# Performance work log

Hardware: AMD Instinct MI355X
Metric: run time of the kernel (lower is better)

Reference implementation:

```python
import jax, jax.numpy as jnp
import numpy as np

EPS = 1e-5
NUM_GROUPS = 8


def setup_inputs() -> dict:
    key = jax.random.key(0)
    ks = jax.random.split(key, 8)
    B, C, H, W = 4, 64, 64, 64
    scale_w = 1.0 / np.sqrt(C)  # roughly xavier scale for [C,C]
    return {
        "x": jax.random.normal(ks[0], (B, C, H, W), dtype=jnp.float32),
        "gamma": jnp.ones((C,), dtype=jnp.float32),
        "beta": jnp.zeros((C,), dtype=jnp.float32),
        "Wq": jax.random.normal(ks[1], (C, C), dtype=jnp.float32) * scale_w,
        "bq": jnp.zeros((C,), dtype=jnp.float32),
        "Wk": jax.random.normal(ks[2], (C, C), dtype=jnp.float32) * scale_w,
        "bk": jnp.zeros((C,), dtype=jnp.float32),
        "Wv": jax.random.normal(ks[3], (C, C), dtype=jnp.float32) * scale_w,
        "bv": jnp.zeros((C,), dtype=jnp.float32),
        "Wp": jax.random.normal(ks[4], (C, C), dtype=jnp.float32) * scale_w,
        "bp": jnp.zeros((C,), dtype=jnp.float32),
    }


def _group_norm(x, gamma, beta):
    # x: [B, C, H, W]; normalize over (C//G, H, W) within each of G groups
    B, C, H, W = x.shape
    xg = x.reshape(B, NUM_GROUPS, -1)
    mean = jnp.mean(xg, axis=-1, keepdims=True)
    var = jnp.var(xg, axis=-1, keepdims=True)
    xn = ((xg - mean) * jax.lax.rsqrt(var + EPS)).reshape(B, C, H, W)
    return xn * gamma[None, :, None, None] + beta[None, :, None, None]


def reference(x, gamma, beta, Wq, bq, Wk, bk, Wv, bv, Wp, bp):
    B, C, H, W = x.shape
    N = H * W
    xn = _group_norm(x, gamma, beta).reshape(B, C, N)  # [B, C, N]
    # 1x1 convs == per-pixel linear maps over channels
    q = jnp.einsum('oc,bcn->bon', Wq, xn) + bq[None, :, None]  # [B, C, N]
    k = jnp.einsum('oc,bcn->bon', Wk, xn) + bk[None, :, None]
    v = jnp.einsum('oc,bcn->bon', Wv, xn) + bv[None, :, None]
    scale = 1.0 / jnp.sqrt(jnp.asarray(C, dtype=x.dtype))
    attn = jnp.einsum('bcn,bcm->bnm', q, k) * scale  # [B, N, N]
    attn = jax.nn.softmax(attn, axis=-1)
    out = jnp.einsum('bnm,bcm->bcn', attn, v)  # [B, C, N]
    out = jnp.einsum('oc,bcn->bon', Wp, out) + bp[None, :, None]
    return x + out.reshape(B, C, H, W)
```

## Files before the change

### kernel.cpp

```cpp
#include <hip/hip_runtime.h>
#include <math.h>

#define B_ 4
#define C_ 64
#define N_ 4096

typedef unsigned short u16;
typedef __attribute__((ext_vector_type(8))) short bf16x8;
typedef __attribute__((ext_vector_type(4))) float f32x4;
typedef __attribute__((ext_vector_type(16))) float f32x16;
typedef __attribute__((ext_vector_type(2))) int i32x2;

__device__ __forceinline__ u16 f2bf(float f) {
    unsigned u = __float_as_uint(f);
    u += 0x7fff + ((u >> 16) & 1);
    return (u16)(u >> 16);
}
__device__ __forceinline__ float bf2f(u16 h) {
    return __uint_as_float(((unsigned)h) << 16);
}

__global__ __launch_bounds__(256) void gn_reduce(const float* __restrict__ x,
                                                 float* __restrict__ partials) {
    int bg = blockIdx.x >> 3, chunk = blockIdx.x & 7;
    const float4* xv = (const float4*)(x + (size_t)bg * 32768 + (size_t)chunk * 4096);
    float s = 0.f, ss = 0.f;
    #pragma unroll
    for (int k = 0; k < 4; k++) {
        float4 v = xv[threadIdx.x + 256 * k];
        s += v.x + v.y + v.z + v.w;
        ss += v.x * v.x + v.y * v.y + v.z * v.z + v.w * v.w;
    }
    #pragma unroll
    for (int off = 1; off < 64; off <<= 1) {
        s += __shfl_xor(s, off);
        ss += __shfl_xor(ss, off);
    }
    __shared__ float red[2][4];
    int w = threadIdx.x >> 6;
    if ((threadIdx.x & 63) == 0) { red[0][w] = s; red[1][w] = ss; }
    __syncthreads();
    if (threadIdx.x == 0) {
        s = red[0][0] + red[0][1] + red[0][2] + red[0][3];
        ss = red[1][0] + red[1][1] + red[1][2] + red[1][3];
        partials[bg * 16 + chunk * 2] = s;
        partials[bg * 16 + chunk * 2 + 1] = ss;
    }
}

__global__ __launch_bounds__(256) void qkv_kernel(
    const float* __restrict__ x, const float* __restrict__ gamma,
    const float* __restrict__ beta, const float* __restrict__ partials,
    const float* __restrict__ Wq, const float* __restrict__ bq,
    const float* __restrict__ Wk, const float* __restrict__ bk,
    const float* __restrict__ Wv, const float* __restrict__ bv,
    u16* __restrict__ Qo, u16* __restrict__ Ko, u16* __restrict__ Vt) {
    __shared__ __align__(16) u16 wt[3][64][64];
    __shared__ __align__(16) u16 xs[64][64];
    __shared__ __align__(16) u16 odt[64][72];

    const int b = blockIdx.x >> 6;
    const int nt = blockIdx.x & 63;
    const int tid = threadIdx.x;
    const float* Ws[3] = {Wq, Wk, Wv};
    const float* bs[3] = {bq, bk, bv};

    {
        const int rw = tid >> 2, qd = tid & 3;
        #pragma unroll
        for (int s = 0; s < 3; s++) {
            const float4* wsrc = (const float4*)(Ws[s] + rw * 64 + qd * 16);
            float4 f0 = wsrc[0], f1 = wsrc[1], f2 = wsrc[2], f3 = wsrc[3];
            u16 pk[16];
            pk[0]=f2bf(f0.x); pk[1]=f2bf(f0.y); pk[2]=f2bf(f0.z); pk[3]=f2bf(f0.w);
            pk[4]=f2bf(f1.x); pk[5]=f2bf(f1.y); pk[6]=f2bf(f1.z); pk[7]=f2bf(f1.w);
            pk[8]=f2bf(f2.x); pk[9]=f2bf(f2.y); pk[10]=f2bf(f2.z); pk[11]=f2bf(f2.w);
            pk[12]=f2bf(f3.x); pk[13]=f2bf(f3.y); pk[14]=f2bf(f3.z); pk[15]=f2bf(f3.w);
            int blk0 = (2 * qd) ^ (rw & 7), blk1 = (2 * qd + 1) ^ (rw & 7);
            *(uint4*)&wt[s][rw][blk0 * 8] = *(uint4*)&pk[0];
            *(uint4*)&wt[s][rw][blk1 * 8] = *(uint4*)&pk[8];
        }
    }
    {
        const int c = tid >> 2, px0 = (tid & 3) * 16;
        const int g = c >> 3, bg = b * 8 + g;
        float s = 0.f, ss = 0.f;
        #pragma unroll
        for (int i = 0; i < 8; i++) {
            s += partials[bg * 16 + i * 2];
            ss += partials[bg * 16 + i * 2 + 1];
        }
        float mean = s * (1.f / 32768.f);
        float var = ss * (1.f / 32768.f) - mean * mean;
        float rstd = rsqrtf(var + 1e-5f);
        float ga = gamma[c] * rstd;
        float bb = beta[c] - mean * ga;
        const float4* xp = (const float4*)(x + ((size_t)(b * 64 + c)) * N_ + nt * 64 + px0);
        float4 q0 = xp[0], q1 = xp[1], q2 = xp[2], q3 = xp[3];
        float vals[16] = {q0.x,q0.y,q0.z,q0.w, q1.x,q1.y,q1.z,q1.w,
                          q2.x,q2.y,q2.z,q2.w, q3.x,q3.y,q3.z,q3.w};
        #pragma unroll
        for (int e = 0; e < 16; e++) {
            int px = px0 + e;
            xs[px][((c >> 3) ^ (px & 7)) * 8 + (c & 7)] = f2bf(vals[e] * ga + bb);
        }
    }
    __syncthreads();

    const int lane = tid & 63, w = tid >> 6;
    const int lr = lane & 15, lg = lane >> 4;
    const f32x4 zz = {0.f, 0.f, 0.f, 0.f};
    const int sa0 = (lg ^ (lr & 7)) * 8, sa1 = ((4 | lg) ^ (lr & 7)) * 8;

    #pragma unroll
    for (int s = 0; s < 3; s++) {
        bf16x8 a0 = *(const bf16x8*)&wt[s][w * 16 + lr][sa0];
        bf16x8 a1 = *(const bf16x8*)&wt[s][w * 16 + lr][sa1];
        float bias[4];
        #pragma unroll
        for (int r = 0; r < 4; r++) bias[r] = bs[s][w * 16 + lg * 4 + r];
        #pragma unroll
        for (int pt = 0; pt < 4; pt++) {
            bf16x8 b0 = *(const bf16x8*)&xs[pt * 16 + lr][sa0];
            bf16x8 b1 = *(const bf16x8*)&xs[pt * 16 + lr][sa1];
            f32x4 acc = __builtin_amdgcn_mfma_f32_16x16x32_bf16(a0, b0, zz, 0, 0, 0);
            acc = __builtin_amdgcn_mfma_f32_16x16x32_bf16(a1, b1, acc, 0, 0, 0);
            if (s == 0) {
                #pragma unroll
                for (int r = 0; r < 4; r++)
                    odt[pt * 16 + lr][w * 16 + lg * 4 + r] = f2bf((acc[r] + bias[r]) * 0.18033688f);
            } else if (s == 1) {
                #pragma unroll
                for (int r = 0; r < 4; r++)
                    odt[pt * 16 + lr][w * 16 + lg * 4 + r] = f2bf(acc[r] + bias[r]);
            } else {
                #pragma unroll
                for (int r = 0; r < 4; r++)
                    odt[w * 16 + lg * 4 + r][pt * 16 + lr] = f2bf(acc[r] + bias[r]);
            }
        }
        __syncthreads();
        if (s < 2) {
            u16* dst = (s == 0 ? Qo : Ko) + ((size_t)(b * N_ + nt * 64)) * 64;
            #pragma unroll
            for (int k2 = 0; k2 < 2; k2++) {
                int c = tid + k2 * 256;
                int px = c >> 3, blk = c & 7;
                *(uint4*)(dst + (size_t)px * 64 + blk * 8) = *(const uint4*)&odt[px][blk * 8];
            }
        } else {
            #pragma unroll
            for (int k2 = 0; k2 < 2; k2++) {
                int c = tid + k2 * 256;
                int co = c >> 3, blk = c & 7;
                *(uint4*)(Vt + ((size_t)(b * 64 + co)) * N_ + nt * 64 + blk * 8) =
                    *(const uint4*)&odt[co][blk * 8];
            }
        }
        __syncthreads();
    }
}

__global__ __launch_bounds__(256, 4) void flash_kernel(
    const u16* __restrict__ Qg, const u16* __restrict__ Kg,
    const u16* __restrict__ Vg, u16* __restrict__ Opart, float* __restrict__ ml,
    int nsplit) {
    __shared__ __align__(16) u16 smem[16384];
    u16* const Ksb0 = smem;
    u16* const Ksb1 = smem + 4096;
    u16* const Vsb0 = smem + 8192;
    u16* const Vsb1 = smem + 12288;

    const int sp = blockIdx.x >> 8;
    const int b  = (blockIdx.x >> 6) & 3;
    const int qt = blockIdx.x & 63;
    const int tid = threadIdx.x;
    const int w = tid >> 6, lane = tid & 63;
    const int l31 = lane & 31, lh = lane >> 5;
    const int qh = w >> 1, kh = w & 1;

    const int per = (nsplit == 4) ? 16 : (nsplit == 3) ? 22 : 32;
    const int kt0 = sp * per;
    const int NT = min(per, 64 - kt0);

    const u16* qptr = Qg + ((size_t)(b * N_ + qt * 64 + qh * 32 + l31)) * 64 + lh * 8;
    bf16x8 q0 = *(const bf16x8*)(qptr);
    bf16x8 q1 = *(const bf16x8*)(qptr + 16);
    bf16x8 q2 = *(const bf16x8*)(qptr + 32);
    bf16x8 q3 = *(const bf16x8*)(qptr + 48);

    const int srow = tid >> 2;
    const int scb  = (tid & 3) * 32;
    const char* Kbase = (const char*)(Kg + (size_t)b * N_ * C_) + (size_t)srow * 128 + scb;
    const char* Vbase = (const char*)(Vg + (size_t)b * C_ * N_) + (size_t)srow * (N_ * 2) + scb;
    const int se0 = srow * 64 + (((scb)      ^ ((srow & 7) << 4)) >> 1);
    const int se1 = srow * 64 + (((scb + 16) ^ ((srow & 7) << 4)) >> 1);

    const int key = kh * 32 + l31;
    int kaoff[4];
    #pragma unroll
    for (int s = 0; s < 4; s++)
        kaoff[s] = key * 64 + (((s * 2 + lh) ^ (key & 7)) << 3);
    int vboff[2][2];
    #pragma unroll
    for (int c = 0; c < 2; c++) {
        int ch = c * 32 + l31;
        #pragma unroll
        for (int s = 0; s < 2; s++)
            vboff[c][s] = ch * 64 + (((kh * 4 + s * 2 + lh) ^ (ch & 7)) << 3);
    }

    {
        uint4 k0a = *(const uint4*)(Kbase + (size_t)kt0 * 8192);
        uint4 k0b = *(const uint4*)(Kbase + (size_t)kt0 * 8192 + 16);
        uint4 v0a = *(const uint4*)(Vbase + kt0 * 128);
        uint4 v0b = *(const uint4*)(Vbase + kt0 * 128 + 16);
        *(uint4*)&Ksb0[se0] = k0a;  *(uint4*)&Ksb0[se1] = k0b;
        *(uint4*)&Vsb0[se0] = v0a;  *(uint4*)&Vsb0[se1] = v0b;
    }
    uint4 ka = *(const uint4*)(Kbase + (size_t)(kt0 + 1) * 8192);
    uint4 kb = *(const uint4*)(Kbase + (size_t)(kt0 + 1) * 8192 + 16);
    uint4 va = *(const uint4*)(Vbase + (kt0 + 1) * 128);
    uint4 vb = *(const uint4*)(Vbase + (kt0 + 1) * 128 + 16);
    __syncthreads();

    f32x16 o0, o1;
    #pragma unroll
    for (int r = 0; r < 16; r++) { o0[r] = 0.f; o1[r] = 0.f; }
    float lsum = 0.f;

    bf16x8 paC0 = {}, paC1 = {};
    bf16x8 vC0 = {}, vC1 = {}, vC2 = {}, vC3 = {};

    for (int t = 0; t < NT; ++t) {
        const int bi = t & 1;
        const u16* ks = bi ? Ksb1 : Ksb0;
        const u16* vs = bi ? Vsb1 : Vsb0;
        u16* kd = bi ? Ksb0 : Ksb1;
        u16* vd = bi ? Vsb0 : Vsb1;

        bf16x8 vN0 = *(const bf16x8*)&vs[vboff[0][0]];
        bf16x8 vN1 = *(const bf16x8*)&vs[vboff[0][1]];
        bf16x8 vN2 = *(const bf16x8*)&vs[vboff[1][0]];
        bf16x8 vN3 = *(const bf16x8*)&vs[vboff[1][1]];

        if (t > 0) {
            __builtin_amdgcn_s_setprio(1);
            o0 = __builtin_amdgcn_mfma_f32_32x32x16_bf16(paC0, vC0, o0, 0, 0, 0);
            o0 = __builtin_amdgcn_mfma_f32_32x32x16_bf16(paC1, vC1, o0, 0, 0, 0);
            o1 = __builtin_amdgcn_mfma_f32_32x32x16_bf16(paC0, vC2, o1, 0, 0, 0);
            o1 = __builtin_amdgcn_mfma_f32_32x32x16_bf16(paC1, vC3, o1, 0, 0, 0);
            __builtin_amdgcn_s_setprio(0);
        }

        f32x16 st;
        #pragma unroll
        for (int r = 0; r < 16; r++) st[r] = 0.f;
        __builtin_amdgcn_s_setprio(1);
        st = __builtin_amdgcn_mfma_f32_32x32x16_bf16(*(const bf16x8*)&ks[kaoff[0]], q0, st, 0, 0, 0);
        st = __builtin_amdgcn_mfma_f32_32x32x16_bf16(*(const bf16x8*)&ks[kaoff[1]], q1, st, 0, 0, 0);
        st = __builtin_amdgcn_mfma_f32_32x32x16_bf16(*(const bf16x8*)&ks[kaoff[2]], q2, st, 0, 0, 0);
        st = __builtin_amdgcn_mfma_f32_32x32x16_bf16(*(const bf16x8*)&ks[kaoff[3]], q3, st, 0, 0, 0);
        __builtin_amdgcn_s_setprio(0);

        #pragma unroll
        for (int r = 0; r < 16; r++) st[r] = exp2f(st[r] - 12.f);
        lsum += (((st[0]+st[1])+(st[2]+st[3])) + ((st[4]+st[5])+(st[6]+st[7])))
              + (((st[8]+st[9])+(st[10]+st[11])) + ((st[12]+st[13])+(st[14]+st[15])));
        unsigned c0,c1,c2,c3,c4,c5,c6,c7;
        asm("v_cvt_pk_bf16_f32 %0, %1, %2" : "=v"(c0) : "v"(st[0]),  "v"(st[1]));
        asm("v_cvt_pk_bf16_f32 %0, %1, %2" : "=v"(c1) : "v"(st[2]),  "v"(st[3]));
        asm("v_cvt_pk_bf16_f32 %0, %1, %2" : "=v"(c2) : "v"(st[4]),  "v"(st[5]));
        asm("v_cvt_pk_bf16_f32 %0, %1, %2" : "=v"(c3) : "v"(st[6]),  "v"(st[7]));
        asm("v_cvt_pk_bf16_f32 %0, %1, %2" : "=v"(c4) : "v"(st[8]),  "v"(st[9]));
        asm("v_cvt_pk_bf16_f32 %0, %1, %2" : "=v"(c5) : "v"(st[10]), "v"(st[11]));
        asm("v_cvt_pk_bf16_f32 %0, %1, %2" : "=v"(c6) : "v"(st[12]), "v"(st[13]));
        asm("v_cvt_pk_bf16_f32 %0, %1, %2" : "=v"(c7) : "v"(st[14]), "v"(st[15]));
        i32x2 r02 = __builtin_amdgcn_permlane32_swap((int)c0, (int)c2, false, false);
        i32x2 r13 = __builtin_amdgcn_permlane32_swap((int)c1, (int)c3, false, false);
        i32x2 r46 = __builtin_amdgcn_permlane32_swap((int)c4, (int)c6, false, false);
        i32x2 r57 = __builtin_amdgcn_permlane32_swap((int)c5, (int)c7, false, false);
        union U { int u[4]; bf16x8 v; };
        U pa0 = {{r02[0], r13[0], r02[1], r13[1]}};
        U pa1 = {{r46[0], r57[0], r46[1], r57[1]}};
        paC0 = pa0.v;
        paC1 = pa1.v;

        if (t < NT - 1) {
            *(uint4*)&kd[se0] = ka;  *(uint4*)&kd[se1] = kb;
            *(uint4*)&vd[se0] = va;  *(uint4*)&vd[se1] = vb;
        }
        __syncthreads();
        if (t < NT - 2) {
            int kt = kt0 + t + 2;
            ka = *(const uint4*)(Kbase + (size_t)kt * 8192);
            kb = *(const uint4*)(Kbase + (size_t)kt * 8192 + 16);
            va = *(const uint4*)(Vbase + kt * 128);
            vb = *(const uint4*)(Vbase + kt * 128 + 16);
        }

        vC0 = vN0; vC1 = vN1; vC2 = vN2; vC3 = vN3;
    }

    o0 = __builtin_amdgcn_mfma_f32_32x32x16_bf16(paC0, vC0, o0, 0, 0, 0);
    o0 = __builtin_amdgcn_mfma_f32_32x32x16_bf16(paC1, vC1, o0, 0, 0, 0);
    o1 = __builtin_amdgcn_mfma_f32_32x32x16_bf16(paC0, vC2, o1, 0, 0, 0);
    o1 = __builtin_amdgcn_mfma_f32_32x32x16_bf16(paC1, vC3, o1, 0, 0, 0);

    float* red = (float*)smem;
    u16* ost = smem + 10240;
    if (kh == 1) {
        float* dst = red + (qh * 64 + lane) * 34;
        #pragma unroll
        for (int r = 0; r < 16; r++) { dst[r] = o0[r]; dst[16 + r] = o1[r]; }
        dst[32] = lsum;
    }
    __syncthreads();
    if (kh == 0) {
        const float* src = red + (qh * 64 + lane) * 34;
        float l2 = lsum + src[32];
        i32x2 rr = __builtin_amdgcn_permlane32_swap(__float_as_int(l2), __float_as_int(l2), false, false);
        float lpart = __int_as_float(lh ? rr[0] : rr[1]);
        float lfull = l2 + lpart;
        #pragma unroll
        for (int r = 0; r < 16; r++) {
            float v0 = o0[r] + src[r];
            float v1 = o1[r] + src[16 + r];
            int ql = qh * 32 + (r & 3) + 8 * (r >> 2) + 4 * lh;
            ost[ql * 64 + l31] = f2bf(v0);
            ost[ql * 64 + 32 + l31] = f2bf(v1);
        }
        if (lane < 32)
            ml[(size_t)sp * 16384 + b * N_ + qt * 64 + qh * 32 + l31] = lfull;
    }
    __syncthreads();
    uint4* op = (uint4*)(Opart + (size_t)sp * 1048576 + ((size_t)(b * N_ + qt * 64)) * 64);
    const uint4* os4 = (const uint4*)ost;
    op[tid] = os4[tid];
    op[tid + 256] = os4[tid + 256];
}

__global__ __launch_bounds__(256) void proj_kernel(
    const u16* __restrict__ Opart, const float* __restrict__ ml,
    const float* __restrict__ Wp, const float* __restrict__ bp,
    const float* __restrict__ x, float* __restrict__ out, int nsplit) {
    __shared__ __align__(16) u16 wp[64][64];
    __shared__ __align__(16) u16 og[64][64];
    const int b = blockIdx.x >> 6;
    const int nt = blockIdx.x & 63;
    const int tid = threadIdx.x;

    {
        const int rw = tid >> 2, qd = tid & 3;
        const float4* wsrc = (const float4*)(Wp + rw * 64 + qd * 16);
        float4 f0 = wsrc[0], f1 = wsrc[1], f2 = wsrc[2], f3 = wsrc[3];
        u16 pk[16];
        pk[0]=f2bf(f0.x); pk[1]=f2bf(f0.y); pk[2]=f2bf(f0.z); pk[3]=f2bf(f0.w);
        pk[4]=f2bf(f1.x); pk[5]=f2bf(f1.y); pk[6]=f2bf(f1.z); pk[7]=f2bf(f1.w);
        pk[8]=f2bf(f2.x); pk[9]=f2bf(f2.y); pk[10]=f2bf(f2.z); pk[11]=f2bf(f2.w);
        pk[12]=f2bf(f3.x); pk[13]=f2bf(f3.y); pk[14]=f2bf(f3.z); pk[15]=f2bf(f3.w);
        int blk0 = (2 * qd) ^ (rw & 7), blk1 = (2 * qd + 1) ^ (rw & 7);
        *(uint4*)&wp[rw][blk0 * 8] = *(uint4*)&pk[0];
        *(uint4*)&wp[rw][blk1 * 8] = *(uint4*)&pk[8];
    }
    {
        #pragma unroll
        for (int k2 = 0; k2 < 2; k2++) {
            int cidx = tid + k2 * 256;
            int px = cidx >> 3, blk = cidx & 7;
            int gpix = b * N_ + nt * 64 + px;
            float lsum = 0.f;
            for (int s = 0; s < nsplit; s++) lsum += ml[(size_t)s * 16384 + gpix];
            float inv = 1.f / lsum;
            float acc8[8] = {0.f,0.f,0.f,0.f,0.f,0.f,0.f,0.f};
            for (int s = 0; s < nsplit; s++) {
                u16 ov[8];
                *(uint4*)ov = *(const uint4*)(Opart + (size_t)s * 1048576 + (size_t)gpix * 64 + blk * 8);
                #pragma unroll
                for (int j = 0; j < 8; j++) acc8[j] += bf2f(ov[j]);
            }
            u16 y[8];
            #pragma unroll
            for (int j = 0; j < 8; j++) y[j] = f2bf(acc8[j] * inv);
            *(uint4*)&og[px][(blk ^ (px & 7)) * 8] = *(uint4*)y;
        }
    }
    __syncthreads();

    const int lane = tid & 63, w = tid >> 6;
    const int lr = lane & 15, lg = lane >> 4;
    const f32x4 zz = {0.f, 0.f, 0.f, 0.f};
    const int sa0 = (lg ^ (lr & 7)) * 8, sa1 = ((4 | lg) ^ (lr & 7)) * 8;

    bf16x8 a0 = *(const bf16x8*)&wp[w * 16 + lr][sa0];
    bf16x8 a1 = *(const bf16x8*)&wp[w * 16 + lr][sa1];
    float bias[4];
    #pragma unroll
    for (int r = 0; r < 4; r++) bias[r] = bp[w * 16 + lg * 4 + r];

    #pragma unroll
    for (int pt = 0; pt < 4; pt++) {
        bf16x8 b0 = *(const bf16x8*)&og[pt * 16 + lr][sa0];
        bf16x8 b1 = *(const bf16x8*)&og[pt * 16 + lr][sa1];
        f32x4 acc = __builtin_amdgcn_mfma_f32_16x16x32_bf16(a0, b0, zz, 0, 0, 0);
        acc = __builtin_amdgcn_mfma_f32_16x16x32_bf16(a1, b1, acc, 0, 0, 0);
        #pragma unroll
        for (int r = 0; r < 4; r++) {
            int cout = w * 16 + lg * 4 + r;
            int px = pt * 16 + lr;
            size_t idx = ((size_t)(b * 64 + cout)) * N_ + nt * 64 + px;
            out[idx] = x[idx] + bias[r] + acc[r];
        }
    }
}

extern "C" void kernel_launch(void* const* d_in, const int* in_sizes, int n_in,
                              void* d_out, int out_size, void* d_ws, size_t ws_size,
                              hipStream_t stream) {
    const float* x     = (const float*)d_in[0];
    const float* gamma = (const float*)d_in[1];
    const float* beta  = (const float*)d_in[2];
    const float* Wq    = (const float*)d_in[3];
    const float* bq    = (const float*)d_in[4];
    const float* Wk    = (const float*)d_in[5];
    const float* bk    = (const float*)d_in[6];
    const float* Wv    = (const float*)d_in[7];
    const float* bv    = (const float*)d_in[8];
    const float* Wp    = (const float*)d_in[9];
    const float* bp    = (const float*)d_in[10];
    float* out = (float*)d_out;

    const size_t elems = (size_t)B_ * N_ * C_;
    const size_t base = 4096 + 262144;
    float* partials = (float*)d_ws;
    float* ml = (float*)((char*)d_ws + 4096);
    u16* Qb = (u16*)((char*)d_ws + base);
    u16* Kb = Qb + elems;
    u16* Vt = Kb + elems;
    u16* Opart = Vt + elems;

    const size_t need4 = base + 3 * elems * 2 + 4 * elems * 2;
    const size_t need3 = base + 3 * elems * 2 + 3 * elems * 2;
    const int nsplit = (ws_size >= need4) ? 4 : (ws_size >= need3) ? 3 : 2;

    gn_reduce<<<256, 256, 0, stream>>>(x, partials);
    qkv_kernel<<<256, 256, 0, stream>>>(x, gamma, beta, partials,
                                        Wq, bq, Wk, bk, Wv, bv, Qb, Kb, Vt);
    flash_kernel<<<nsplit * 256, 256, 0, stream>>>(Qb, Kb, Vt, Opart, ml, nsplit);
    proj_kernel<<<256, 256, 0, stream>>>(Opart, ml, Wp, bp, x, out, nsplit);
}
```

Before: 56.17 us.

## Pre-swizzle K/V into MFMA fragment order and load directly from global

The QKV kernel now writes K and V in a per-tile layout that matches the MFMA operand fragment order, so each lane's bf16x8 operand sits contiguously in global memory. The flash kernel drops the LDS double buffer, swizzle and per-iteration __syncthreads, loads K and V fragments straight into registers, and prefetches the next K tile. The PV MFMAs are no longer deferred by one iteration. This removes LDS traffic and block barriers, but each wave pair now reads K/V tiles redundantly from global or L2 and relies on the cache to hide latency. The K prefetch on the last iteration also reads one tile past the split's range.

```diff
diff --git a/kernel.cpp b/kernel.cpp
--- a/kernel.cpp
+++ b/kernel.cpp
@@ -54,7 +54,7 @@
     const float* __restrict__ Wq, const float* __restrict__ bq,
     const float* __restrict__ Wk, const float* __restrict__ bk,
     const float* __restrict__ Wv, const float* __restrict__ bv,
-    u16* __restrict__ Qo, u16* __restrict__ Ko, u16* __restrict__ Vt) {
+    u16* __restrict__ Qo, u16* __restrict__ Kf, u16* __restrict__ Vf) {
     __shared__ __align__(16) u16 wt[3][64][64];
     __shared__ __align__(16) u16 xs[64][64];
     __shared__ __align__(16) u16 odt[64][72];
@@ -140,36 +140,43 @@
             }
         }
         __syncthreads();
-        if (s < 2) {
-            u16* dst = (s == 0 ? Qo : Ko) + ((size_t)(b * N_ + nt * 64)) * 64;
+        if (s == 0) {
+            u16* dst = Qo + ((size_t)(b * N_ + nt * 64)) * 64;
             #pragma unroll
             for (int k2 = 0; k2 < 2; k2++) {
                 int c = tid + k2 * 256;
                 int px = c >> 3, blk = c & 7;
                 *(uint4*)(dst + (size_t)px * 64 + blk * 8) = *(const uint4*)&odt[px][blk * 8];
             }
-        } else {
+        } else if (s == 1) {
+            u16* dst = Kf + ((size_t)(b * 64 + nt)) * 4096;
             #pragma unroll
             for (int k2 = 0; k2 < 2; k2++) {
-                int c = tid + k2 * 256;
-                int co = c >> 3, blk = c & 7;
-                *(uint4*)(Vt + ((size_t)(b * 64 + co)) * N_ + nt * 64 + blk * 8) =
-                    *(const uint4*)&odt[co][blk * 8];
+                int f = tid + k2 * 256;
+                int khf = f >> 8, sf = (f >> 6) & 3, lhf = (f >> 5) & 1, l31f = f & 31;
+                *(uint4*)(dst + (size_t)f * 8) =
+                    *(const uint4*)&odt[khf * 32 + l31f][(sf * 2 + lhf) * 8];
             }
+        } else {
+            u16* dst = Vf + ((size_t)(b * 64 + nt)) * 4096;
+            #pragma unroll
+            for (int k2 = 0; k2 < 2; k2++) {
+                int f = tid + k2 * 256;
+                int khf = f >> 8, cf = (f >> 7) & 1, s2f = (f >> 6) & 1;
+                int lhf = (f >> 5) & 1, l31f = f & 31;
+                *(uint4*)(dst + (size_t)f * 8) =
+                    *(const uint4*)&odt[cf * 32 + l31f][(khf * 4 + s2f * 2 + lhf) * 8];
+            }
         }
         __syncthreads();
     }
 }
 
 __global__ __launch_bounds__(256, 4) void flash_kernel(
-    const u16* __restrict__ Qg, const u16* __restrict__ Kg,
-    const u16* __restrict__ Vg, u16* __restrict__ Opart, float* __restrict__ ml,
+    const u16* __restrict__ Qg, const u16* __restrict__ Kf,
+    const u16* __restrict__ Vf, u16* __restrict__ Opart, float* __restrict__ ml,
     int nsplit) {
-    __shared__ __align__(16) u16 smem[16384];
-    u16* const Ksb0 = smem;
-    u16* const Ksb1 = smem + 4096;
-    u16* const Vsb0 = smem + 8192;
-    u16* const Vsb1 = smem + 12288;
+    __shared__ __align__(16) u16 smem[14336];
 
     const int sp = blockIdx.x >> 8;
     const int b  = (blockIdx.x >> 6) & 3;
@@ -189,79 +196,41 @@
     bf16x8 q2 = *(const bf16x8*)(qptr + 32);
     bf16x8 q3 = *(const bf16x8*)(qptr + 48);
 
-    const int srow = tid >> 2;
-    const int scb  = (tid & 3) * 32;
-    const char* Kbase = (const char*)(Kg + (size_t)b * N_ * C_) + (size_t)srow * 128 + scb;
-    const char* Vbase = (const char*)(Vg + (size_t)b * C_ * N_) + (size_t)srow * (N_ * 2) + scb;
-    const int se0 = srow * 64 + (((scb)      ^ ((srow & 7) << 4)) >> 1);
-    const int se1 = srow * 64 + (((scb + 16) ^ ((srow & 7) << 4)) >> 1);
-
-    const int key = kh * 32 + l31;
-    int kaoff[4];
-    #pragma unroll
-    for (int s = 0; s < 4; s++)
-        kaoff[s] = key * 64 + (((s * 2 + lh) ^ (key & 7)) << 3);
-    int vboff[2][2];
-    #pragma unroll
-    for (int c = 0; c < 2; c++) {
-        int ch = c * 32 + l31;
-        #pragma unroll
-        for (int s = 0; s < 2; s++)
-            vboff[c][s] = ch * 64 + (((kh * 4 + s * 2 + lh) ^ (ch & 7)) << 3);
-    }
-
-    {
-        uint4 k0a = *(const uint4*)(Kbase + (size_t)kt0 * 8192);
-        uint4 k0b = *(const uint4*)(Kbase + (size_t)kt0 * 8192 + 16);
-        uint4 v0a = *(const uint4*)(Vbase + kt0 * 128);
-        uint4 v0b = *(const uint4*)(Vbase + kt0 * 128 + 16);
-        *(uint4*)&Ksb0[se0] = k0a;  *(uint4*)&Ksb0[se1] = k0b;
-        *(uint4*)&Vsb0[se0] = v0a;  *(uint4*)&Vsb0[se1] = v0b;
-    }
-    uint4 ka = *(const uint4*)(Kbase + (size_t)(kt0 + 1) * 8192);
-    uint4 kb = *(const uint4*)(Kbase + (size_t)(kt0 + 1) * 8192 + 16);
-    uint4 va = *(const uint4*)(Vbase + (kt0 + 1) * 128);
-    uint4 vb = *(const uint4*)(Vbase + (kt0 + 1) * 128 + 16);
-    __syncthreads();
+    const u16* kp = Kf + ((size_t)(b * 64 + kt0)) * 4096 + kh * 2048 + lane * 8;
+    const u16* vp = Vf + ((size_t)(b * 64 + kt0)) * 4096 + kh * 2048 + lane * 8;
+
+    bf16x8 kf0 = *(const bf16x8*)(kp);
+    bf16x8 kf1 = *(const bf16x8*)(kp + 512);
+    bf16x8 kf2 = *(const bf16x8*)(kp + 1024);
+    bf16x8 kf3 = *(const bf16x8*)(kp + 1536);
 
     f32x16 o0, o1;
     #pragma unroll
     for (int r = 0; r < 16; r++) { o0[r] = 0.f; o1[r] = 0.f; }
     float lsum = 0.f;
 
-    bf16x8 paC0 = {}, paC1 = {};
-    bf16x8 vC0 = {}, vC1 = {}, vC2 = {}, vC3 = {};
-
     for (int t = 0; t < NT; ++t) {
-        const int bi = t & 1;
-        const u16* ks = bi ? Ksb1 : Ksb0;
-        const u16* vs = bi ? Vsb1 : Vsb0;
-        u16* kd = bi ? Ksb0 : Ksb1;
-        u16* vd = bi ? Vsb0 : Vsb1;
-
-        bf16x8 vN0 = *(const bf16x8*)&vs[vboff[0][0]];
-        bf16x8 vN1 = *(const bf16x8*)&vs[vboff[0][1]];
-        bf16x8 vN2 = *(const bf16x8*)&vs[vboff[1][0]];
-        bf16x8 vN3 = *(const bf16x8*)&vs[vboff[1][1]];
-
-        if (t > 0) {
-            __builtin_amdgcn_s_setprio(1);
-            o0 = __builtin_amdgcn_mfma_f32_32x32x16_bf16(paC0, vC0, o0, 0, 0, 0);
-            o0 = __builtin_amdgcn_mfma_f32_32x32x16_bf16(paC1, vC1, o0, 0, 0, 0);
-            o1 = __builtin_amdgcn_mfma_f32_32x32x16_bf16(paC0, vC2, o1, 0, 0, 0);
-            o1 = __builtin_amdgcn_mfma_f32_32x32x16_bf16(paC1, vC3, o1, 0, 0, 0);
-            __builtin_amdgcn_s_setprio(0);
-        }
+        const u16* vtp = vp + (size_t)t * 4096;
+        bf16x8 vf0 = *(const bf16x8*)(vtp);
+        bf16x8 vf1 = *(const bf16x8*)(vtp + 512);
+        bf16x8 vf2 = *(const bf16x8*)(vtp + 1024);
+        bf16x8 vf3 = *(const bf16x8*)(vtp + 1536);
 
         f32x16 st;
         #pragma unroll
         for (int r = 0; r < 16; r++) st[r] = 0.f;
         __builtin_amdgcn_s_setprio(1);
-        st = __builtin_amdgcn_mfma_f32_32x32x16_bf16(*(const bf16x8*)&ks[kaoff[0]], q0, st, 0, 0, 0);
-        st = __builtin_amdgcn_mfma_f32_32x32x16_bf16(*(const bf16x8*)&ks[kaoff[1]], q1, st, 0, 0, 0);
-        st = __builtin_amdgcn_mfma_f32_32x32x16_bf16(*(const bf16x8*)&ks[kaoff[2]], q2, st, 0, 0, 0);
-        st = __builtin_amdgcn_mfma_f32_32x32x16_bf16(*(const bf16x8*)&ks[kaoff[3]], q3, st, 0, 0, 0);
+        st = __builtin_amdgcn_mfma_f32_32x32x16_bf16(kf0, q0, st, 0, 0, 0);
+        st = __builtin_amdgcn_mfma_f32_32x32x16_bf16(kf1, q1, st, 0, 0, 0);
+        st = __builtin_amdgcn_mfma_f32_32x32x16_bf16(kf2, q2, st, 0, 0, 0);
+        st = __builtin_amdgcn_mfma_f32_32x32x16_bf16(kf3, q3, st, 0, 0, 0);
         __builtin_amdgcn_s_setprio(0);
+
+        const u16* knp = kp + (size_t)(t + 1) * 4096;
+        kf0 = *(const bf16x8*)(knp);
+        kf1 = *(const bf16x8*)(knp + 512);
+        kf2 = *(const bf16x8*)(knp + 1024);
+        kf3 = *(const bf16x8*)(knp + 1536);
 
         #pragma unroll
         for (int r = 0; r < 16; r++) st[r] = exp2f(st[r] - 12.f);
@@ -283,29 +252,14 @@
         union U { int u[4]; bf16x8 v; };
         U pa0 = {{r02[0], r13[0], r02[1], r13[1]}};
         U pa1 = {{r46[0], r57[0], r46[1], r57[1]}};
-        paC0 = pa0.v;
-        paC1 = pa1.v;
-
-        if (t < NT - 1) {
-            *(uint4*)&kd[se0] = ka;  *(uint4*)&kd[se1] = kb;
-            *(uint4*)&vd[se0] = va;  *(uint4*)&vd[se1] = vb;
-        }
-        __syncthreads();
-        if (t < NT - 2) {
-            int kt = kt0 + t + 2;
-            ka = *(const uint4*)(Kbase + (size_t)kt * 8192);
-            kb = *(const uint4*)(Kbase + (size_t)kt * 8192 + 16);
-            va = *(const uint4*)(Vbase + kt * 128);
-            vb = *(const uint4*)(Vbase + kt * 128 + 16);
-        }
-
-        vC0 = vN0; vC1 = vN1; vC2 = vN2; vC3 = vN3;
-    }
-
-    o0 = __builtin_amdgcn_mfma_f32_32x32x16_bf16(paC0, vC0, o0, 0, 0, 0);
-    o0 = __builtin_amdgcn_mfma_f32_32x32x16_bf16(paC1, vC1, o0, 0, 0, 0);
-    o1 = __builtin_amdgcn_mfma_f32_32x32x16_bf16(paC0, vC2, o1, 0, 0, 0);
-    o1 = __builtin_amdgcn_mfma_f32_32x32x16_bf16(paC1, vC3, o1, 0, 0, 0);
+
+        __builtin_amdgcn_s_setprio(1);
+        o0 = __builtin_amdgcn_mfma_f32_32x32x16_bf16(pa0.v, vf0, o0, 0, 0, 0);
+        o0 = __builtin_amdgcn_mfma_f32_32x32x16_bf16(pa1.v, vf1, o0, 0, 0, 0);
+        o1 = __builtin_amdgcn_mfma_f32_32x32x16_bf16(pa0.v, vf2, o1, 0, 0, 0);
+        o1 = __builtin_amdgcn_mfma_f32_32x32x16_bf16(pa1.v, vf3, o1, 0, 0, 0);
+        __builtin_amdgcn_s_setprio(0);
+    }
 
     float* red = (float*)smem;
     u16* ost = smem + 10240;
```

Result: faster. 52.31 us (-6.9%).
